# Kernel optimization log

Hardware: AMD Instinct MI355X
Metric: run time of the kernel (lower is better)

Reference implementation:

```python
import jax, jax.numpy as jnp
import numpy as np
import math

HIDDEN = 256
GUMBEL_EPS = 1e-20
MASK_EPS = 1e-8
TAU = 1.0


def _gumbel(u):
    return -jnp.log(-jnp.log(u + GUMBEL_EPS) + GUMBEL_EPS)


def setup_inputs() -> dict:
    key = jax.random.key(0)
    ks = jax.random.split(key, 16)
    B, N = 16, 128
    goal_dim, obs_dim, local_dim, num_skills = 64, 128, 64, 16
    h = HIDDEN

    def lin(k, out_d, in_d):
        kw, kb = jax.random.split(k)
        bound = 1.0 / math.sqrt(in_d)
        W = jax.random.uniform(kw, (out_d, in_d), minval=-bound, maxval=bound, dtype=jnp.float32)
        b = jax.random.uniform(kb, (out_d,), minval=-bound, maxval=bound, dtype=jnp.float32)
        return W, b

    Wq, bq = lin(ks[0], h, goal_dim)
    Wk, bk = lin(ks[1], h, obs_dim)
    Wv, bv = lin(ks[2], h, obs_dim)
    Wo, bo = lin(ks[3], h, h)
    Ws, bs = lin(ks[4], num_skills, local_dim + goal_dim + h)

    return {
        "goals": jax.random.normal(ks[5], (B, N, goal_dim), dtype=jnp.float32),
        "agents": jax.random.normal(ks[6], (B, N, obs_dim), dtype=jnp.float32),
        "agents_local": jax.random.normal(ks[7], (B, N, local_dim), dtype=jnp.float32),
        "u1": jax.random.uniform(ks[8], (B, N, N), dtype=jnp.float32),
        "u2": jax.random.uniform(ks[9], (B, N, N), dtype=jnp.float32),
        "Wq": Wq, "bq": bq, "Wk": Wk, "bk": bk, "Wv": Wv, "bv": bv,
        "Wo": Wo, "bo": bo, "Ws": Ws, "bs": bs,
    }


def reference(goals, agents, agents_local, u1, u2, Wq, bq, Wk, bk, Wv, bv, Wo, bo, Ws, bs):
    # Projections
    Q = jnp.einsum('bnd,hd->bnh', goals, Wq) + bq   # [B,N,h]
    K = jnp.einsum('bmd,hd->bmh', agents, Wk) + bk  # [B,N,h]
    V = jnp.einsum('bmd,hd->bmh', agents, Wv) + bv  # [B,N,h]

    scale = math.sqrt(HIDDEN) + 1e-12
    logits = jnp.einsum('bnh,bmh->bnm', Q, K) / scale  # [B,N,N]

    # Gumbel-sigmoid mask (soft, hard=False)
    g1, g2 = _gumbel(u1), _gumbel(u2)
    mask = jax.nn.sigmoid((logits + g1 - g2) / TAU)  # [B,N,N]

    scores = logits + jnp.log(mask + MASK_EPS)
    attn = jax.nn.softmax(scores, axis=-1)  # [B,N,N]

    # info[b,n,h] = sum_m attn[b,n,m] * mask[b,n,m] * V[b,m,h]
    # (equivalent to (attn.unsqueeze(-1) * V_masked).sum(dim=2) without
    #  materializing the [B,N,N,h] V_masked tensor)
    info = jnp.einsum('bnm,bnm,bmh->bnh', attn, mask, V)

    out = jnp.einsum('bnh,gh->bng', info, Wo) + bo  # [B,N,h]

    concat = jnp.concatenate([agents_local, goals, out], axis=-1)
    logit = jnp.einsum('bnc,sc->bns', concat, Ws) + bs  # [B,N,num_skills]

    return (logit, mask, attn, out)
```

## Files before the change

### kernel.cpp

```cpp
#include <hip/hip_runtime.h>
#include <math.h>


typedef float f32x4 __attribute__((ext_vector_type(4)));
typedef short s16x8 __attribute__((ext_vector_type(8)));

#define WOBF_OFF  0
#define QBF_OFF   32768
#define KBF_OFF   294912
#define VTBF_OFF  557056

#define LOGIT_OFF 0
#define MASK_OFF  32768
#define ATTN_OFF  294912
#define OUT_OFF   557056

static __device__ __forceinline__ unsigned short f2bf(float x) {
  unsigned int u = __float_as_uint(x);
  u = (u + 0x7fffu + ((u >> 16) & 1u)) >> 16;
  return (unsigned short)u;
}
static __device__ __forceinline__ float bf2f(unsigned short h) {
  return __uint_as_float(((unsigned int)h) << 16);
}

static __device__ __forceinline__ void split8(const float* __restrict__ p,
                                              s16x8* hi, s16x8* lo) {
  float4 x0 = *(const float4*)p;
  float4 x1 = *(const float4*)(p + 4);
  float xs[8] = {x0.x, x0.y, x0.z, x0.w, x1.x, x1.y, x1.z, x1.w};
#pragma unroll
  for (int j = 0; j < 8; j++) {
    unsigned short h = f2bf(xs[j]);
    (*hi)[j] = (short)h;
    (*lo)[j] = (short)f2bf(xs[j] - bf2f(h));
  }
}
#define MFMA(a, b, c) __builtin_amdgcn_mfma_f32_16x16x32_bf16((a), (b), (c), 0, 0, 0)

__global__ __launch_bounds__(512) void proj_k(
    const float* __restrict__ goals, const float* __restrict__ agents,
    const float* __restrict__ Wq, const float* __restrict__ bq,
    const float* __restrict__ Wk, const float* __restrict__ bk,
    const float* __restrict__ Wv, const float* __restrict__ bv,
    const float* __restrict__ Wo, float* __restrict__ ws) {
  unsigned short* qbf  = (unsigned short*)(ws + QBF_OFF);
  unsigned short* kbf  = (unsigned short*)(ws + KBF_OFF);
  unsigned short* vtbf = (unsigned short*)(ws + VTBF_OFF);
  unsigned short* wobf = (unsigned short*)(ws + WOBF_OFF);

  __shared__ __align__(16) float xg[16 * 68];
  __shared__ __align__(16) float xa[16 * 132];

  int t = threadIdx.x;
  int bid = blockIdx.x;
  int xcd = bid & 7, j = bid >> 3;
  int bb = 2 * xcd + (j & 1);
  int sub = j >> 1;
  int r0 = bb * 128 + (sub >> 1) * 16;
  int colbase = (sub & 1) * 128;

  for (int i = t; i < 1024; i += 512) xg[(i >> 6) * 68 + (i & 63)] = goals[(size_t)r0 * 64 + i];
  for (int i = t; i < 2048; i += 512) xa[(i >> 7) * 132 + (i & 127)] = agents[(size_t)r0 * 128 + i];
  if (t < 256) {
    int jj = bid * 256 + t;
    wobf[jj] = f2bf(Wo[jj]);
  }
  __syncthreads();

  int w = t >> 6, l = t & 63, lr = l & 15, lc = l >> 4;
  int oc = colbase + w * 16 + lr;

  {
    f32x4 acc = {0.f, 0.f, 0.f, 0.f};
#pragma unroll
    for (int kk = 0; kk < 2; kk++) {
      s16x8 ahi, alo, bhi, blo;
      split8(&xg[lr * 68 + kk * 32 + lc * 8], &ahi, &alo);
      split8(&Wq[(size_t)oc * 64 + kk * 32 + lc * 8], &bhi, &blo);
      acc = MFMA(ahi, bhi, acc);
      acc = MFMA(alo, bhi, acc);
      acc = MFMA(ahi, blo, acc);
    }
    float bqv = bq[oc];
#pragma unroll
    for (int q = 0; q < 4; q++)
      qbf[(size_t)(r0 + 4 * lc + q) * 256 + oc] = f2bf(acc[q] + bqv);
  }
  {
    f32x4 acc = {0.f, 0.f, 0.f, 0.f};
#pragma unroll
    for (int kk = 0; kk < 4; kk++) {
      s16x8 ahi, alo, bhi, blo;
      split8(&xa[lr * 132 + kk * 32 + lc * 8], &ahi, &alo);
      split8(&Wk[(size_t)oc * 128 + kk * 32 + lc * 8], &bhi, &blo);
      acc = MFMA(ahi, bhi, acc);
      acc = MFMA(alo, bhi, acc);
      acc = MFMA(ahi, blo, acc);
    }
    float bkv = bk[oc];
#pragma unroll
    for (int q = 0; q < 4; q++)
      kbf[(size_t)(r0 + 4 * lc + q) * 256 + oc] = f2bf(acc[q] + bkv);
  }
  {
    f32x4 acc = {0.f, 0.f, 0.f, 0.f};
#pragma unroll
    for (int kk = 0; kk < 4; kk++) {
      s16x8 ahi, alo, bhi, blo;
      split8(&xa[lr * 132 + kk * 32 + lc * 8], &ahi, &alo);
      split8(&Wv[(size_t)oc * 128 + kk * 32 + lc * 8], &bhi, &blo);
      acc = MFMA(ahi, bhi, acc);
      acc = MFMA(alo, bhi, acc);
      acc = MFMA(ahi, blo, acc);
    }
    float bvv = bv[oc];
    int m0 = r0 & 127;
#pragma unroll
    for (int q = 0; q < 4; q++)
      vtbf[(size_t)(bb * 256 + oc) * 128 + m0 + 4 * lc + q] = f2bf(acc[q] + bvv);
  }
}

__global__ __launch_bounds__(1024) void attn_k(
    const float* __restrict__ goals, const float* __restrict__ agents_local,
    const float* __restrict__ u1, const float* __restrict__ u2,
    const float* __restrict__ bo, const float* __restrict__ Wsm,
    const float* __restrict__ bs, const float* __restrict__ ws,
    float* __restrict__ out) {
  const unsigned short* Qbf  = (const unsigned short*)(ws + QBF_OFF);
  const unsigned short* Kbf  = (const unsigned short*)(ws + KBF_OFF);
  const unsigned short* VTbf = (const unsigned short*)(ws + VTBF_OFF);
  const unsigned short* Wobf = (const unsigned short*)(ws + WOBF_OFF);
  float* o_logit = out + LOGIT_OFF;
  float* o_mask  = out + MASK_OFF;
  float* o_attn  = out + ATTN_OFF;
  float* o_out   = out + OUT_OFF;

  int bid = blockIdx.x;
  int xcd = bid & 7, idx = bid >> 3;
  int b  = 2 * xcd + (idx & 1);
  int n0 = (idx >> 1) << 3;
  int rtile = n0 & 0x70;
  int soff  = n0 & 8;
  int t = threadIdx.x;
  int w = t >> 6, l = t & 63, lr = l & 15, lc = l >> 4;

  __shared__ __align__(16) float Spp[2][8][132];
  __shared__ __align__(16) unsigned short Wb[16 * 136];
  __shared__ __align__(16) unsigned short Ib[16 * 264];
  __shared__ __align__(16) float outb[8 * 260];
  __shared__ __align__(16) float Wsb[16 * 384];
  __shared__ __align__(16) float cgb[8 * 128];
  __shared__ float redmax[8][2], redsum[8][2];

#pragma unroll
  for (int i = 0; i < 6; i++) Wsb[t + i * 1024] = Wsm[t + i * 1024];
  {
    int r = t >> 7, c = t & 127;
    int row = b * 128 + n0 + r;
    cgb[r * 128 + c] = (c < 64) ? agents_local[(size_t)row * 64 + c]
                                : goals[(size_t)row * 64 + (c - 64)];
  }

  int pm = t & 127, prl = t >> 7;
  int prow = b * 128 + n0 + prl;
  float uu1 = __builtin_nontemporal_load(&u1[(size_t)prow * 128 + pm]);
  float uu2 = __builtin_nontemporal_load(&u2[(size_t)prow * 128 + pm]);
  int h0g = w * 16;
  float bov = bo[h0g + lr];
  float bsv = bs[(t >> 3) & 15];
  const s16x8* vtp = (const s16x8*)(VTbf + (size_t)(b * 256 + h0g + lr) * 128);
  s16x8 fv0 = vtp[lc], fv1 = vtp[4 + lc], fv2 = vtp[8 + lc], fv3 = vtp[12 + lc];
  const s16x8* wop = (const s16x8*)(Wobf + (size_t)(h0g + lr) * 256);
  s16x8 fo0 = wop[lc],      fo1 = wop[4 + lc],  fo2 = wop[8 + lc],  fo3 = wop[12 + lc];
  s16x8 fo4 = wop[16 + lc], fo5 = wop[20 + lc], fo6 = wop[24 + lc], fo7 = wop[28 + lc];

  {
    int mt = w & 7, kh = w >> 3;
    const s16x8* ap = (const s16x8*)(Qbf + (size_t)(b * 128 + rtile + lr) * 256 + kh * 128);
    const s16x8* bp = (const s16x8*)(Kbf + (size_t)(b * 128 + mt * 16 + lr) * 256 + kh * 128);
    f32x4 acc = {0.f, 0.f, 0.f, 0.f};
#pragma unroll
    for (int kk = 0; kk < 4; kk++)
      acc = MFMA(ap[kk * 4 + lc], bp[kk * 4 + lc], acc);
    if ((lc >> 1) == (soff >> 3)) {
#pragma unroll
      for (int q = 0; q < 4; q++) Spp[kh][(4 * lc + q) & 7][mt * 16 + lr] = acc[q];
    }
    if (t < 544) ((unsigned int*)(Wb + (soff ^ 8) * 136))[t] = 0u;
  }
  __syncthreads();

  {
    int half = (t >> 6) & 1;
    float lg = (Spp[0][prl][pm] + Spp[1][prl][pm]) * 0.0625f;
    float g1 = -__logf(-__logf(uu1 + 1e-20f) + 1e-20f);
    float g2 = -__logf(-__logf(uu2 + 1e-20f) + 1e-20f);
    float mkv = 1.0f / (1.0f + __expf(-(lg + g1 - g2)));
    __builtin_nontemporal_store(mkv, &o_mask[(size_t)prow * 128 + pm]);
    float sc = lg + __logf(mkv + 1e-8f);
    float v = sc;
#pragma unroll
    for (int off = 32; off >= 1; off >>= 1) v = fmaxf(v, __shfl_xor(v, off));
    if (l == 0) redmax[prl][half] = v;
    __syncthreads();
    float rmax = fmaxf(redmax[prl][0], redmax[prl][1]);
    float e = __expf(sc - rmax);
    float s = e;
#pragma unroll
    for (int off = 32; off >= 1; off >>= 1) s += __shfl_xor(s, off);
    if (l == 0) redsum[prl][half] = s;
    __syncthreads();
    float rsum = redsum[prl][0] + redsum[prl][1];
    float attn = e / rsum;
    __builtin_nontemporal_store(attn, &o_attn[(size_t)prow * 128 + pm]);
    Wb[(soff + prl) * 136 + pm] = f2bf(attn * mkv);
  }
  __syncthreads();

  {
    s16x8 a0 = *(const s16x8*)(Wb + lr * 136 + 0 * 32 + lc * 8);
    s16x8 a1 = *(const s16x8*)(Wb + lr * 136 + 1 * 32 + lc * 8);
    s16x8 a2 = *(const s16x8*)(Wb + lr * 136 + 2 * 32 + lc * 8);
    s16x8 a3 = *(const s16x8*)(Wb + lr * 136 + 3 * 32 + lc * 8);
    f32x4 acc = {0.f, 0.f, 0.f, 0.f};
    acc = MFMA(a0, fv0, acc);
    acc = MFMA(a1, fv1, acc);
    acc = MFMA(a2, fv2, acc);
    acc = MFMA(a3, fv3, acc);
#pragma unroll
    for (int q = 0; q < 4; q++) Ib[(4 * lc + q) * 264 + h0g + lr] = f2bf(acc[q]);
  }
  __syncthreads();

  {
    f32x4 acc = {0.f, 0.f, 0.f, 0.f};
    acc = MFMA(*(const s16x8*)(Ib + lr * 264 + 0 * 32 + lc * 8), fo0, acc);
    acc = MFMA(*(const s16x8*)(Ib + lr * 264 + 1 * 32 + lc * 8), fo1, acc);
    acc = MFMA(*(const s16x8*)(Ib + lr * 264 + 2 * 32 + lc * 8), fo2, acc);
    acc = MFMA(*(const s16x8*)(Ib + lr * 264 + 3 * 32 + lc * 8), fo3, acc);
    acc = MFMA(*(const s16x8*)(Ib + lr * 264 + 4 * 32 + lc * 8), fo4, acc);
    acc = MFMA(*(const s16x8*)(Ib + lr * 264 + 5 * 32 + lc * 8), fo5, acc);
    acc = MFMA(*(const s16x8*)(Ib + lr * 264 + 6 * 32 + lc * 8), fo6, acc);
    acc = MFMA(*(const s16x8*)(Ib + lr * 264 + 7 * 32 + lc * 8), fo7, acc);
    if ((lc >> 1) == (soff >> 3)) {
#pragma unroll
      for (int q = 0; q < 4; q++) {
        int rloc = (4 * lc + q) & 7;
        float val = acc[q] + bov;
        __builtin_nontemporal_store(val, &o_out[(size_t)(b * 128 + n0 + rloc) * 256 + h0g + lr]);
        outb[rloc * 260 + h0g + lr] = val;
      }
    }
  }
  __syncthreads();

  {
    int rloc = t >> 7, s = (t >> 3) & 15, p = t & 7;
    int row = b * 128 + n0 + rloc;
    const float* wsr = &Wsb[s * 384];
    float acc = 0.f;
#pragma unroll
    for (int i = 0; i < 12; i++) {
      int cc = p * 48 + i * 4;
      float4 c4;
      if (cc < 128) c4 = *(const float4*)&cgb[rloc * 128 + cc];
      else          c4 = *(const float4*)&outb[rloc * 260 + (cc - 128)];
      float4 w4 = *(const float4*)&wsr[cc];
      acc = fmaf(w4.x, c4.x, fmaf(w4.y, c4.y, fmaf(w4.z, c4.z, fmaf(w4.w, c4.w, acc))));
    }
    acc += __shfl_xor(acc, 1);
    acc += __shfl_xor(acc, 2);
    acc += __shfl_xor(acc, 4);
    if (p == 0) __builtin_nontemporal_store(acc + bsv, &o_logit[row * 16 + s]);
  }
}

extern "C" void kernel_launch(void* const* d_in, const int* in_sizes, int n_in,
                              void* d_out, int out_size, void* d_ws, size_t ws_size,
                              hipStream_t stream) {
  const float* goals        = (const float*)d_in[0];
  const float* agents       = (const float*)d_in[1];
  const float* agents_local = (const float*)d_in[2];
  const float* u1           = (const float*)d_in[3];
  const float* u2           = (const float*)d_in[4];
  const float* Wq = (const float*)d_in[5];
  const float* bq = (const float*)d_in[6];
  const float* Wk = (const float*)d_in[7];
  const float* bk = (const float*)d_in[8];
  const float* Wv = (const float*)d_in[9];
  const float* bv = (const float*)d_in[10];
  const float* Wo = (const float*)d_in[11];
  const float* bo = (const float*)d_in[12];
  const float* Wsm = (const float*)d_in[13];
  const float* bs  = (const float*)d_in[14];
  float* out = (float*)d_out;
  float* ws  = (float*)d_ws;

  proj_k<<<256, 512, 0, stream>>>(goals, agents, Wq, bq, Wk, bk, Wv, bv, Wo, ws);
  attn_k<<<256, 1024, 0, stream>>>(goals, agents_local, u1, u2, bo, Wsm, bs, ws, out);
}
```

Measured before the change: 27.47 us.

## Compute each softmax row in one wavefront and merge K/V projection loops

The softmax stage now gives each of the first 8 wavefronts one full 128-wide row, with two elements per lane and float2 loads and stores. Row max and sum become pure wave shuffles, which removes two block-wide __syncthreads and the shared reduction arrays. Half the waves sit idle during this stage, and the non-temporal hints on the u1/u2/mask/attn traffic are dropped. The projection kernel also fuses the K and V loops so the split of the shared input tile is done once.

Result: no change. 27.23 us (median of 2 runs) (-0.9%).

```diff
diff --git a/kernel.cpp b/kernel.cpp
--- a/kernel.cpp
+++ b/kernel.cpp
@@ -88,37 +88,29 @@
       qbf[(size_t)(r0 + 4 * lc + q) * 256 + oc] = f2bf(acc[q] + bqv);
   }
   {
-    f32x4 acc = {0.f, 0.f, 0.f, 0.f};
+    f32x4 accK = {0.f, 0.f, 0.f, 0.f};
+    f32x4 accV = {0.f, 0.f, 0.f, 0.f};
 #pragma unroll
     for (int kk = 0; kk < 4; kk++) {
-      s16x8 ahi, alo, bhi, blo;
+      s16x8 ahi, alo;
       split8(&xa[lr * 132 + kk * 32 + lc * 8], &ahi, &alo);
-      split8(&Wk[(size_t)oc * 128 + kk * 32 + lc * 8], &bhi, &blo);
-      acc = MFMA(ahi, bhi, acc);
-      acc = MFMA(alo, bhi, acc);
-      acc = MFMA(ahi, blo, acc);
-    }
-    float bkv = bk[oc];
-#pragma unroll
-    for (int q = 0; q < 4; q++)
-      kbf[(size_t)(r0 + 4 * lc + q) * 256 + oc] = f2bf(acc[q] + bkv);
-  }
-  {
-    f32x4 acc = {0.f, 0.f, 0.f, 0.f};
-#pragma unroll
-    for (int kk = 0; kk < 4; kk++) {
-      s16x8 ahi, alo, bhi, blo;
-      split8(&xa[lr * 132 + kk * 32 + lc * 8], &ahi, &alo);
-      split8(&Wv[(size_t)oc * 128 + kk * 32 + lc * 8], &bhi, &blo);
-      acc = MFMA(ahi, bhi, acc);
-      acc = MFMA(alo, bhi, acc);
-      acc = MFMA(ahi, blo, acc);
-    }
-    float bvv = bv[oc];
+      s16x8 bhiK, bloK, bhiV, bloV;
+      split8(&Wk[(size_t)oc * 128 + kk * 32 + lc * 8], &bhiK, &bloK);
+      split8(&Wv[(size_t)oc * 128 + kk * 32 + lc * 8], &bhiV, &bloV);
+      accK = MFMA(ahi, bhiK, accK);
+      accK = MFMA(alo, bhiK, accK);
+      accK = MFMA(ahi, bloK, accK);
+      accV = MFMA(ahi, bhiV, accV);
+      accV = MFMA(alo, bhiV, accV);
+      accV = MFMA(ahi, bloV, accV);
+    }
+    float bkv = bk[oc], bvv = bv[oc];
     int m0 = r0 & 127;
 #pragma unroll
-    for (int q = 0; q < 4; q++)
-      vtbf[(size_t)(bb * 256 + oc) * 128 + m0 + 4 * lc + q] = f2bf(acc[q] + bvv);
+    for (int q = 0; q < 4; q++) {
+      kbf[(size_t)(r0 + 4 * lc + q) * 256 + oc] = f2bf(accK[q] + bkv);
+      vtbf[(size_t)(bb * 256 + oc) * 128 + m0 + 4 * lc + q] = f2bf(accV[q] + bvv);
+    }
   }
 }
 
@@ -152,7 +144,6 @@
   __shared__ __align__(16) float outb[8 * 260];
   __shared__ __align__(16) float Wsb[16 * 384];
   __shared__ __align__(16) float cgb[8 * 128];
-  __shared__ float redmax[8][2], redsum[8][2];
 
 #pragma unroll
   for (int i = 0; i < 6; i++) Wsb[t + i * 1024] = Wsm[t + i * 1024];
@@ -163,10 +154,12 @@
                                 : goals[(size_t)row * 64 + (c - 64)];
   }
 
-  int pm = t & 127, prl = t >> 7;
-  int prow = b * 128 + n0 + prl;
-  float uu1 = __builtin_nontemporal_load(&u1[(size_t)prow * 128 + pm]);
-  float uu2 = __builtin_nontemporal_load(&u2[(size_t)prow * 128 + pm]);
+  float2 uu1v = make_float2(0.f, 0.f), uu2v = make_float2(0.f, 0.f);
+  if (w < 8) {
+    int srow = b * 128 + n0 + w;
+    uu1v = *(const float2*)&u1[(size_t)srow * 128 + 2 * l];
+    uu2v = *(const float2*)&u2[(size_t)srow * 128 + 2 * l];
+  }
   int h0g = w * 16;
   float bov = bo[h0g + lr];
   float bsv = bs[(t >> 3) & 15];
@@ -192,30 +185,31 @@
   }
   __syncthreads();
 
-  {
-    int half = (t >> 6) & 1;
-    float lg = (Spp[0][prl][pm] + Spp[1][prl][pm]) * 0.0625f;
-    float g1 = -__logf(-__logf(uu1 + 1e-20f) + 1e-20f);
-    float g2 = -__logf(-__logf(uu2 + 1e-20f) + 1e-20f);
-    float mkv = 1.0f / (1.0f + __expf(-(lg + g1 - g2)));
-    __builtin_nontemporal_store(mkv, &o_mask[(size_t)prow * 128 + pm]);
-    float sc = lg + __logf(mkv + 1e-8f);
-    float v = sc;
+  if (w < 8) {
+    int m0 = 2 * l;
+    int row = b * 128 + n0 + w;
+    float lg0 = (Spp[0][w][m0]     + Spp[1][w][m0])     * 0.0625f;
+    float lg1 = (Spp[0][w][m0 + 1] + Spp[1][w][m0 + 1]) * 0.0625f;
+    float g10 = -__logf(-__logf(uu1v.x + 1e-20f) + 1e-20f);
+    float g20 = -__logf(-__logf(uu2v.x + 1e-20f) + 1e-20f);
+    float g11 = -__logf(-__logf(uu1v.y + 1e-20f) + 1e-20f);
+    float g21 = -__logf(-__logf(uu2v.y + 1e-20f) + 1e-20f);
+    float mk0 = 1.0f / (1.0f + __expf(-(lg0 + g10 - g20)));
+    float mk1 = 1.0f / (1.0f + __expf(-(lg1 + g11 - g21)));
+    *(float2*)&o_mask[(size_t)row * 128 + m0] = make_float2(mk0, mk1);
+    float sc0 = lg0 + __logf(mk0 + 1e-8f);
+    float sc1 = lg1 + __logf(mk1 + 1e-8f);
+    float v = fmaxf(sc0, sc1);
 #pragma unroll
     for (int off = 32; off >= 1; off >>= 1) v = fmaxf(v, __shfl_xor(v, off));
-    if (l == 0) redmax[prl][half] = v;
-    __syncthreads();
-    float rmax = fmaxf(redmax[prl][0], redmax[prl][1]);
-    float e = __expf(sc - rmax);
-    float s = e;
+    float e0 = __expf(sc0 - v), e1 = __expf(sc1 - v);
+    float s = e0 + e1;
 #pragma unroll
     for (int off = 32; off >= 1; off >>= 1) s += __shfl_xor(s, off);
-    if (l == 0) redsum[prl][half] = s;
-    __syncthreads();
-    float rsum = redsum[prl][0] + redsum[prl][1];
-    float attn = e / rsum;
-    __builtin_nontemporal_store(attn, &o_attn[(size_t)prow * 128 + pm]);
-    Wb[(soff + prl) * 136 + pm] = f2bf(attn * mkv);
+    float at0 = e0 / s, at1 = e1 / s;
+    *(float2*)&o_attn[(size_t)row * 128 + m0] = make_float2(at0, at1);
+    Wb[(soff + w) * 136 + m0]     = f2bf(at0 * mk0);
+    Wb[(soff + w) * 136 + m0 + 1] = f2bf(at1 * mk1);
   }
   __syncthreads();
 
```
